# Optimization experiments

Measured on AMD Instinct MI355X. Metric: run time of the kernel, lower is better.

## Reference

```python
import jax, jax.numpy as jnp
import numpy as np

B, N, T, CIN, COUT, K, DIL = 8, 207, 12, 64, 64, 3, 1


def setup_inputs() -> dict:
    key = jax.random.key(0)
    ks = jax.random.split(key, 13)
    s = 0.05
    return {
        "X": jax.random.normal(ks[0], (B, N, T, CIN), jnp.float32),
        "wA": jax.random.normal(ks[1], (COUT, CIN, 1, K), jnp.float32) * s,
        "bA": jax.random.normal(ks[2], (COUT,), jnp.float32) * s,
        "wB": jax.random.normal(ks[3], (COUT, CIN, 1, K), jnp.float32) * s,
        "bB": jax.random.normal(ks[4], (COUT,), jnp.float32) * s,
        "wq": jax.random.normal(ks[5], (COUT // 8, COUT), jnp.float32) * s,
        "bq": jax.random.normal(ks[6], (COUT // 8,), jnp.float32) * s,
        "wk": jax.random.normal(ks[7], (COUT // 8, COUT), jnp.float32) * s,
        "bk": jax.random.normal(ks[8], (COUT // 8,), jnp.float32) * s,
        "wv": jax.random.normal(ks[9], (COUT, COUT), jnp.float32) * s,
        "bv": jax.random.normal(ks[10], (COUT,), jnp.float32) * s,
        "gamma": jax.random.normal(ks[11], (1,), jnp.float32) * 0.1,
    }


def reference(X, wA, bA, wB, bB, wq, bq, wk, bk, wv, bv, gamma):
    # X: [B, N, T, C] -> [B, C, N, T]
    x = jnp.transpose(X, (0, 3, 1, 2))
    k_size = wA.shape[-1]
    pad = (k_size - 1) * DIL  # causal left pad == pad-both + drop-right in torch code

    def causal_conv(w, b):
        y = jax.lax.conv_general_dilated(
            x, w, window_strides=(1, 1),
            padding=((0, 0), (pad, 0)),
            rhs_dilation=(1, DIL),
            dimension_numbers=("NCHW", "OIHW", "NCHW"))
        return y + b[None, :, None, None]

    A = causal_conv(wA, bA)
    Bg = causal_conv(wB, bB)
    h = A * jax.nn.sigmoid(Bg)  # [B, C, N, T]

    b_, c, w_, h_ = h.shape
    L = w_ * h_
    h2 = h.reshape(b_, c, L)  # [B, C, L]
    q = jnp.einsum("oc,bcl->bol", wq, h2) + bq[None, :, None]  # [B, C/8, L]
    kk = jnp.einsum("oc,bcl->bol", wk, h2) + bk[None, :, None]
    v = jnp.einsum("oc,bcl->bol", wv, h2) + bv[None, :, None]   # [B, C, L]

    energy = jnp.einsum("bql,bqm->blm", q, kk)  # [B, L, L]
    attn = jax.nn.softmax(energy, axis=-1)
    out = jnp.einsum("bcm,blm->bcl", v, attn).reshape(b_, c, w_, h_)
    out = gamma[0] * out + h
    return jnp.transpose(out, (0, 2, 3, 1))  # [B, N, T, C]
```

## Files before the change

### kernel.cpp

```cpp
#include <hip/hip_runtime.h>
#include <hip/hip_bf16.h>

#define Bn 8
#define Nn 207
#define Tn 12
#define Cn 64
#define Ln (Nn*Tn)
#define LP 2496
#define NT 39
#define NB 104

typedef unsigned int u32;
typedef unsigned short u16;
typedef _Float16 f16;
typedef __attribute__((ext_vector_type(4))) _Float16 half4;
typedef __attribute__((ext_vector_type(4))) float floatx4;

__device__ __forceinline__ u16 f2h(float f) { f16 h = (f16)f; return *(u16*)&h; }
__device__ __forceinline__ float h2f_lo(u32 u) { u16 x = (u16)u;        f16 h = *(f16*)&x; return (float)h; }
__device__ __forceinline__ float h2f_hi(u32 u) { u16 x = (u16)(u >> 16); f16 h = *(f16*)&x; return (float)h; }

#define W_PW   0
#define U_WVT  24576
#define F_WK   14336
#define F_WQ   14848
#define U_K    30720
#define U_Q    190464
#define U_HT   350208

__global__ __launch_bounds__(256) void prep_kernel(
    const float* __restrict__ wA, const float* __restrict__ wB,
    const float* __restrict__ wq, const float* __restrict__ wk,
    const float* __restrict__ wv, float* __restrict__ ws)
{
    u16* wsu = (u16*)ws;
    u32* wsw = (u32*)ws;
    int idx = blockIdx.x * 256 + threadIdx.x;
    if (idx < 12288) {
        int co = idx & 63, j = (idx >> 6) & 7, cig = (idx >> 9) & 7, k = idx >> 12;
        int src = (co*64 + cig*8 + j)*3 + k;
        wsw[W_PW + idx] = (u32)f2h(wA[src]) | ((u32)f2h(wB[src]) << 16);
    } else if (idx < 16384) {
        int j = idx - 12288;
        wsu[U_WVT + j] = f2h(wv[j]);
    } else if (idx < 16896) {
        int j = idx - 16384; int o = j & 7, c = j >> 3;
        ws[F_WK + j] = wk[o*Cn + c];
    } else if (idx < 17408) {
        int j = idx - 16896; int o = j & 7, c = j >> 3;
        ws[F_WQ + j] = wq[o*Cn + c];
    } else if (idx < 18944) {
        int j = idx - 17408;
        int b = j / 192, rem = j - b*192;
        int which = rem / 96, rr = rem - which*96;
        wsu[(which ? U_Q : U_K) + (size_t)b*LP*8 + Ln*8 + rr] = 0;
    } else if (idx < 25088) {
        int j = idx - 18944;
        int b = j / 768, rem = j - b*768;
        int c = rem / 12, mm = 52 + (rem - c*12);
        int ss = mm >> 4, q = (mm >> 2) & 3, i = mm & 3;
        int cs = c >> 4, rm = c & 15;
        wsu[U_HT + (size_t)b*NT*4096 + ((38*16 + ss*4 + cs)*256 + (rm*4 + q)*4 + i)] = 0;
    }
}

__global__ __launch_bounds__(256, 2) void conv_k_kernel(
    const float* __restrict__ X,
    const float* __restrict__ bA, const float* __restrict__ bB,
    const float* __restrict__ bk, const float* __restrict__ bq,
    float* __restrict__ ws, float* __restrict__ out)
{
    __shared__ u32   w_s[12288];
    __shared__ float xs[Tn*Cn];
    __shared__ float hs[Tn*Cn];
    __shared__ float wkq_s[1024];
    int b = blockIdx.x & 7;
    int n = blockIdx.x >> 3;
    int tid = threadIdx.x;

    for (int i = tid; i < 3072; i += 256)
        ((uint4*)w_s)[i] = ((const uint4*)ws)[i];
    const float* Xp = X + (size_t)(b*Nn + n)*Tn*Cn;
    for (int i = tid; i < (Tn*Cn)/4; i += 256)
        ((float4*)xs)[i] = ((const float4*)Xp)[i];
    ((float4*)wkq_s)[tid] = ((const float4*)(ws + F_WK))[tid];
    __syncthreads();

    int co = tid & 63;
    int tg = tid >> 6;
    float aA[3] = {bA[co], bA[co], bA[co]};
    float aB[3] = {bB[co], bB[co], bB[co]};
    int tb = tg*3 - 2;

    #pragma unroll 1
    for (int cig = 0; cig < 8; ++cig) {
        float xr[5][8];
        #pragma unroll
        for (int d = 0; d < 5; ++d) {
            int tp = tb + d;
            if (tp >= 0) {
                float4 xa = *(const float4*)(xs + tp*Cn + cig*8);
                float4 xb = *(const float4*)(xs + tp*Cn + cig*8 + 4);
                xr[d][0]=xa.x; xr[d][1]=xa.y; xr[d][2]=xa.z; xr[d][3]=xa.w;
                xr[d][4]=xb.x; xr[d][5]=xb.y; xr[d][6]=xb.z; xr[d][7]=xb.w;
            } else {
                #pragma unroll
                for (int j = 0; j < 8; ++j) xr[d][j] = 0.f;
            }
        }
        #pragma unroll
        for (int k = 0; k < 3; ++k) {
            #pragma unroll
            for (int j = 0; j < 8; ++j) {
                u32 p = w_s[((k*8 + cig)*8 + j)*64 + co];
                float wa = h2f_lo(p), wb = h2f_hi(p);
                #pragma unroll
                for (int tt = 0; tt < 3; ++tt) {
                    aA[tt] += xr[tt + k][j] * wa;
                    aB[tt] += xr[tt + k][j] * wb;
                }
            }
        }
    }

    #pragma unroll
    for (int tt = 0; tt < 3; ++tt) {
        int t = tg*3 + tt;
        float hv = aA[tt] * (1.f / (1.f + __expf(-aB[tt])));
        hs[t*Cn + co] = hv;
        out[((size_t)b*Ln + (size_t)n*Tn + t)*Cn + co] = hv;
    }
    __syncthreads();

    if (tid < 96) {
        int r = tid >> 3, o = tid & 7;
        float acc = bk[o];
        for (int c = 0; c < Cn; ++c) acc += hs[r*Cn + c] * wkq_s[c*8 + o];
        ((u16*)ws)[U_K + (size_t)b*LP*8 + ((size_t)n*Tn + r)*8 + o] = f2h(acc);
    } else if (tid < 192) {
        int r = (tid - 96) >> 3, o = tid & 7;
        float acc = bq[o];
        for (int c = 0; c < Cn; ++c) acc += hs[r*Cn + c] * wkq_s[512 + c*8 + o];
        ((u16*)ws)[U_Q + (size_t)b*LP*8 + ((size_t)n*Tn + r)*8 + o] = f2h(acc);
    }
    {
        int jj = tid >> 6, c = tid & 63;
        if (jj < 3) {
            int m = n*Tn + 4*jj;
            int tile = m >> 6, mloc = m & 63;
            int ss = mloc >> 4, q = (mloc >> 2) & 3;
            int cs = c >> 4, rm = c & 15;
            u32 p0 = ((u32)f2h(hs[(4*jj+1)*Cn + c]) << 16) | f2h(hs[(4*jj+0)*Cn + c]);
            u32 p1 = ((u32)f2h(hs[(4*jj+3)*Cn + c]) << 16) | f2h(hs[(4*jj+2)*Cn + c]);
            u16* ht = (u16*)ws + U_HT + (size_t)b*NT*4096
                    + ((tile*16 + ss*4 + cs)*256 + (rm*4 + q)*4);
            *(uint2*)ht = make_uint2(p0, p1);
        }
    }
}

__global__ __launch_bounds__(256, 3) void attn_kernel(
    const float* __restrict__ gamma, const float* __restrict__ bv,
    const float* __restrict__ ws, float* __restrict__ out)
{
    __shared__ float part[4*64*24];
    __shared__ float den_part[4][32];

    int b  = blockIdx.x & 7;
    int nb = blockIdx.x >> 3;
    int R0 = nb*24;
    int tid = threadIdx.x;
    int lane = tid & 63;
    int w = tid >> 6;
    int rm = lane & 15;
    int quad = lane >> 4;

    const u16* wsu = (const u16*)ws;
    const u16* kb = wsu + U_K  + (size_t)b*LP*8;
    const u16* qb = wsu + U_Q  + (size_t)b*LP*8;
    const u16* hb = wsu + U_HT + (size_t)b*NT*4096;

    half4 qf0, qf1;
    {
        uint2 u0 = make_uint2(0, 0), u1 = make_uint2(0, 0);
        int r0 = R0 + rm;       if (r0 >= LP) r0 = LP - 1;
        int r1 = R0 + 16 + rm;  if (r1 >= LP) r1 = LP - 1;
        if (quad < 2) {
            u0 = *(const uint2*)(qb + (size_t)r0*8 + 4*quad);
            u1 = *(const uint2*)(qb + (size_t)r1*8 + 4*quad);
        }
        qf0 = *(half4*)&u0; qf1 = *(half4*)&u1;
    }

    floatx4 acc[4][2];
    #pragma unroll
    for (int cs = 0; cs < 4; ++cs)
        #pragma unroll
        for (int g = 0; g < 2; ++g) acc[cs][g] = (floatx4){0.f, 0.f, 0.f, 0.f};
    float dsum0 = 0.f, dsum1 = 0.f;

    uint2 k0_0,k0_1,k0_2,k0_3, k1_0,k1_1,k1_2,k1_3;
    uint2 h0_0,h0_1,h0_2,h0_3,h0_4,h0_5,h0_6,h0_7,h0_8,h0_9,h0_10,h0_11,h0_12,h0_13,h0_14,h0_15;
    uint2 h1_0,h1_1,h1_2,h1_3,h1_4,h1_5,h1_6,h1_7,h1_8,h1_9,h1_10,h1_11,h1_12,h1_13,h1_14,h1_15;

#define LDK(kt, SS) ((quad < 2) ? *(const uint2*)((kt) + ((SS)*16 + rm)*8 + 4*quad) : make_uint2(0,0))
#define LDH(ht, IDX) (*(const uint2*)((ht) + (IDX)*256 + lane*4))

#define LOADT(B, T) {                                                          \
    int tc = ((T) < NT) ? (T) : (NT-1);                                        \
    const u16* kt_ = kb + (size_t)tc*512;                                      \
    const u16* ht_ = hb + (size_t)tc*4096;                                     \
    k##B##_0 = LDK(kt_, 0); k##B##_1 = LDK(kt_, 1);                            \
    k##B##_2 = LDK(kt_, 2); k##B##_3 = LDK(kt_, 3);                            \
    h##B##_0  = LDH(ht_, 0);  h##B##_1  = LDH(ht_, 1);                         \
    h##B##_2  = LDH(ht_, 2);  h##B##_3  = LDH(ht_, 3);                         \
    h##B##_4  = LDH(ht_, 4);  h##B##_5  = LDH(ht_, 5);                         \
    h##B##_6  = LDH(ht_, 6);  h##B##_7  = LDH(ht_, 7);                         \
    h##B##_8  = LDH(ht_, 8);  h##B##_9  = LDH(ht_, 9);                         \
    h##B##_10 = LDH(ht_, 10); h##B##_11 = LDH(ht_, 11);                        \
    h##B##_12 = LDH(ht_, 12); h##B##_13 = LDH(ht_, 13);                        \
    h##B##_14 = LDH(ht_, 14); h##B##_15 = LDH(ht_, 15);                        \
}

#define COMPSS(KR, HA, HB_, HC, HD, T, SS) {                                   \
    half4 kf = *(half4*)&KR;                                                   \
    floatx4 s0 = {0.f,0.f,0.f,0.f}, s1 = {0.f,0.f,0.f,0.f};                    \
    s0 = __builtin_amdgcn_mfma_f32_16x16x16f16(kf, qf0, s0, 0, 0, 0);          \
    s1 = __builtin_amdgcn_mfma_f32_16x16x16f16(kf, qf1, s1, 0, 0, 0);          \
    half4 e0, e1;                                                              \
    int mb = (T)*64 + (SS)*16 + 4*quad;                                        \
    _Pragma("unroll")                                                          \
    for (int i_ = 0; i_ < 4; ++i_) {                                           \
        float ev0 = (mb + i_ < Ln) ? __expf(s0[i_]) : 0.f;                     \
        float ev1 = (mb + i_ < Ln) ? __expf(s1[i_]) : 0.f;                     \
        dsum0 += ev0; dsum1 += ev1;                                            \
        e0[i_] = (f16)ev0; e1[i_] = (f16)ev1;                                  \
    }                                                                          \
    half4 a0_ = *(half4*)&HA, a1_ = *(half4*)&HB_, a2_ = *(half4*)&HC, a3_ = *(half4*)&HD; \
    acc[0][0] = __builtin_amdgcn_mfma_f32_16x16x16f16(a0_, e0, acc[0][0], 0, 0, 0); \
    acc[0][1] = __builtin_amdgcn_mfma_f32_16x16x16f16(a0_, e1, acc[0][1], 0, 0, 0); \
    acc[1][0] = __builtin_amdgcn_mfma_f32_16x16x16f16(a1_, e0, acc[1][0], 0, 0, 0); \
    acc[1][1] = __builtin_amdgcn_mfma_f32_16x16x16f16(a1_, e1, acc[1][1], 0, 0, 0); \
    acc[2][0] = __builtin_amdgcn_mfma_f32_16x16x16f16(a2_, e0, acc[2][0], 0, 0, 0); \
    acc[2][1] = __builtin_amdgcn_mfma_f32_16x16x16f16(a2_, e1, acc[2][1], 0, 0, 0); \
    acc[3][0] = __builtin_amdgcn_mfma_f32_16x16x16f16(a3_, e0, acc[3][0], 0, 0, 0); \
    acc[3][1] = __builtin_amdgcn_mfma_f32_16x16x16f16(a3_, e1, acc[3][1], 0, 0, 0); \
}

#define COMPT(B, T) {                                                          \
    COMPSS(k##B##_0, h##B##_0,  h##B##_1,  h##B##_2,  h##B##_3,  T, 0)         \
    COMPSS(k##B##_1, h##B##_4,  h##B##_5,  h##B##_6,  h##B##_7,  T, 1)         \
    COMPSS(k##B##_2, h##B##_8,  h##B##_9,  h##B##_10, h##B##_11, T, 2)         \
    COMPSS(k##B##_3, h##B##_12, h##B##_13, h##B##_14, h##B##_15, T, 3)         \
}

    LOADT(0, w)
    for (int i = 0; i < 5; ++i) {
        int t0 = w + 8*i;
        LOADT(1, t0 + 4)
        COMPT(0, t0)
        LOADT(0, t0 + 8)
        COMPT(1, t0 + 4)
    }
#undef LOADT
#undef COMPT
#undef COMPSS
#undef LDK
#undef LDH

    {
        float s_ = dsum0;
        s_ += __shfl_xor(s_, 16, 64);
        s_ += __shfl_xor(s_, 32, 64);
        if (quad == 0) den_part[w][rm] = s_;
        float t_ = dsum1;
        t_ += __shfl_xor(t_, 16, 64);
        t_ += __shfl_xor(t_, 32, 64);
        if (quad == 0) den_part[w][16 + rm] = t_;
    }

    float* pw = part + w*1536;
    #pragma unroll
    for (int cs = 0; cs < 4; ++cs) {
        #pragma unroll
        for (int i = 0; i < 4; ++i)
            pw[(cs*16 + quad*4 + i)*24 + rm] = acc[cs][0][i];
        if (rm < 8) {
            #pragma unroll
            for (int i = 0; i < 4; ++i)
                pw[(cs*16 + quad*4 + i)*24 + 16 + rm] = acc[cs][1][i];
        }
    }
    __syncthreads();

    for (int j = tid; j < 1536; j += 256)
        part[j] = part[j] + part[1536 + j] + part[3072 + j] + part[4608 + j];
    __syncthreads();

    int o = tid & 63, rq = tid >> 6;
    float gam = gamma[0];
    float bvo = bv[o];
    const u16* wvr = wsu + U_WVT + o*64;
    uint4 wvu[8];
    #pragma unroll
    for (int x = 0; x < 8; ++x) wvu[x] = *(const uint4*)(wvr + x*8);
    #pragma unroll
    for (int rr = 0; rr < 6; ++rr) {
        int r = rq*6 + rr;
        int row = R0 + r;
        if (row < Ln) {
            float den = den_part[0][r] + den_part[1][r] + den_part[2][r] + den_part[3][r];
            float p = 0.f;
            #pragma unroll
            for (int x = 0; x < 8; ++x) {
                const f16* hh = (const f16*)&wvu[x];
                #pragma unroll
                for (int i = 0; i < 8; ++i)
                    p += (float)hh[i] * part[(x*8 + i)*24 + r];
            }
            size_t gi = ((size_t)b*Ln + row)*64 + o;
            out[gi] = gam*(bvo + p/den) + out[gi];
        }
    }
}

extern "C" void kernel_launch(void* const* d_in, const int* in_sizes, int n_in,
                              void* d_out, int out_size, void* d_ws, size_t ws_size,
                              hipStream_t stream) {
    const float* X     = (const float*)d_in[0];
    const float* wA    = (const float*)d_in[1];
    const float* bA    = (const float*)d_in[2];
    const float* wB    = (const float*)d_in[3];
    const float* bB    = (const float*)d_in[4];
    const float* wq    = (const float*)d_in[5];
    const float* bq    = (const float*)d_in[6];
    const float* wk    = (const float*)d_in[7];
    const float* bk    = (const float*)d_in[8];
    const float* wv    = (const float*)d_in[9];
    const float* bv    = (const float*)d_in[10];
    const float* gamma = (const float*)d_in[11];
    float* out = (float*)d_out;
    float* ws  = (float*)d_ws;

    prep_kernel<<<98, 256, 0, stream>>>(wA, wB, wq, wk, wv, ws);
    conv_k_kernel<<<Bn*Nn, 256, 0, stream>>>(X, bA, bB, bk, bq, ws, out);
    attn_kernel<<<Bn*NB, 256, 0, stream>>>(gamma, bv, ws, out);
}
```

Measured before the change: 158.6 us.

## Stream conv weights from global, drop LDS staging, widen attention blocks to 8 waves

The conv kernel no longer copies the full 48KB packed weight table into shared memory per block. It reads weights directly from global or cache in a per-thread contiguous layout, double-buffered across input-channel groups, and the prep kernel is reordered to write that layout. This lowers LDS use so the launch bound can allow 4 blocks per CU. The attention kernel moves to 512 threads (8 waves), each wave covering 5 key tiles instead of 10, with a wider partial-sum reduction in shared memory; this raises parallelism per block but uses more LDS and adds reduction work.

```diff
diff --git a/kernel.cpp b/kernel.cpp
--- a/kernel.cpp
+++ b/kernel.cpp
@@ -37,9 +37,10 @@
     u32* wsw = (u32*)ws;
     int idx = blockIdx.x * 256 + threadIdx.x;
     if (idx < 12288) {
-        int co = idx & 63, j = (idx >> 6) & 7, cig = (idx >> 9) & 7, k = idx >> 12;
+        int j = idx & 7, co = (idx >> 3) & 63, cig = (idx >> 9) & 7, k = idx >> 12;
         int src = (co*64 + cig*8 + j)*3 + k;
-        wsw[W_PW + idx] = (u32)f2h(wA[src]) | ((u32)f2h(wB[src]) << 16);
+        wsw[W_PW + ((k*8 + cig)*64 + co)*8 + j] =
+            (u32)f2h(wA[src]) | ((u32)f2h(wB[src]) << 16);
     } else if (idx < 16384) {
         int j = idx - 12288;
         wsu[U_WVT + j] = f2h(wv[j]);
@@ -64,13 +65,12 @@
     }
 }
 
-__global__ __launch_bounds__(256, 2) void conv_k_kernel(
+__global__ __launch_bounds__(256, 4) void conv_k_kernel(
     const float* __restrict__ X,
     const float* __restrict__ bA, const float* __restrict__ bB,
     const float* __restrict__ bk, const float* __restrict__ bq,
     float* __restrict__ ws, float* __restrict__ out)
 {
-    __shared__ u32   w_s[12288];
     __shared__ float xs[Tn*Cn];
     __shared__ float hs[Tn*Cn];
     __shared__ float wkq_s[1024];
@@ -78,8 +78,6 @@
     int n = blockIdx.x >> 3;
     int tid = threadIdx.x;
 
-    for (int i = tid; i < 3072; i += 256)
-        ((uint4*)w_s)[i] = ((const uint4*)ws)[i];
     const float* Xp = X + (size_t)(b*Nn + n)*Tn*Cn;
     for (int i = tid; i < (Tn*Cn)/4; i += 256)
         ((float4*)xs)[i] = ((const float4*)Xp)[i];
@@ -91,37 +89,64 @@
     float aA[3] = {bA[co], bA[co], bA[co]};
     float aB[3] = {bB[co], bB[co], bB[co]};
     int tb = tg*3 - 2;
-
+    const uint4* wp4 = (const uint4*)((const u32*)ws + W_PW);
+
+    uint4 p00, p01, p02, p03, p04, p05;
+    uint4 p10, p11, p12, p13, p14, p15;
+
+#define LOADW(V0,V1,V2,V3,V4,V5, CIG) {                    \
+    V0 = wp4[(0*8 + (CIG))*128 + co*2 + 0];                \
+    V1 = wp4[(0*8 + (CIG))*128 + co*2 + 1];                \
+    V2 = wp4[(1*8 + (CIG))*128 + co*2 + 0];                \
+    V3 = wp4[(1*8 + (CIG))*128 + co*2 + 1];                \
+    V4 = wp4[(2*8 + (CIG))*128 + co*2 + 0];                \
+    V5 = wp4[(2*8 + (CIG))*128 + co*2 + 1];                \
+}
+
+#define COMPK(K, WH0, WH1) {                               \
+    u32 uu[8] = {WH0.x, WH0.y, WH0.z, WH0.w,               \
+                 WH1.x, WH1.y, WH1.z, WH1.w};              \
+    _Pragma("unroll")                                      \
+    for (int j = 0; j < 8; ++j) {                          \
+        float wav = h2f_lo(uu[j]), wbv = h2f_hi(uu[j]);    \
+        _Pragma("unroll")                                  \
+        for (int tt = 0; tt < 3; ++tt) {                   \
+            aA[tt] += xr[tt + K][j] * wav;                 \
+            aB[tt] += xr[tt + K][j] * wbv;                 \
+        }                                                  \
+    }                                                      \
+}
+
+#define COMPC(CIG, V0,V1,V2,V3,V4,V5) {                    \
+    float xr[5][8];                                        \
+    _Pragma("unroll")                                      \
+    for (int d = 0; d < 5; ++d) {                          \
+        int tp = tb + d;                                   \
+        if (tp >= 0) {                                     \
+            float4 xa = *(const float4*)(xs + tp*Cn + (CIG)*8);     \
+            float4 xb = *(const float4*)(xs + tp*Cn + (CIG)*8 + 4); \
+            xr[d][0]=xa.x; xr[d][1]=xa.y; xr[d][2]=xa.z; xr[d][3]=xa.w; \
+            xr[d][4]=xb.x; xr[d][5]=xb.y; xr[d][6]=xb.z; xr[d][7]=xb.w; \
+        } else {                                           \
+            _Pragma("unroll")                              \
+            for (int j = 0; j < 8; ++j) xr[d][j] = 0.f;    \
+        }                                                  \
+    }                                                      \
+    COMPK(0, V0, V1) COMPK(1, V2, V3) COMPK(2, V4, V5)     \
+}
+
+    LOADW(p00,p01,p02,p03,p04,p05, 0)
     #pragma unroll 1
-    for (int cig = 0; cig < 8; ++cig) {
-        float xr[5][8];
-        #pragma unroll
-        for (int d = 0; d < 5; ++d) {
-            int tp = tb + d;
-            if (tp >= 0) {
-                float4 xa = *(const float4*)(xs + tp*Cn + cig*8);
-                float4 xb = *(const float4*)(xs + tp*Cn + cig*8 + 4);
-                xr[d][0]=xa.x; xr[d][1]=xa.y; xr[d][2]=xa.z; xr[d][3]=xa.w;
-                xr[d][4]=xb.x; xr[d][5]=xb.y; xr[d][6]=xb.z; xr[d][7]=xb.w;
-            } else {
-                #pragma unroll
-                for (int j = 0; j < 8; ++j) xr[d][j] = 0.f;
-            }
-        }
-        #pragma unroll
-        for (int k = 0; k < 3; ++k) {
-            #pragma unroll
-            for (int j = 0; j < 8; ++j) {
-                u32 p = w_s[((k*8 + cig)*8 + j)*64 + co];
-                float wa = h2f_lo(p), wb = h2f_hi(p);
-                #pragma unroll
-                for (int tt = 0; tt < 3; ++tt) {
-                    aA[tt] += xr[tt + k][j] * wa;
-                    aB[tt] += xr[tt + k][j] * wb;
-                }
-            }
-        }
-    }
+    for (int c2 = 0; c2 < 4; ++c2) {
+        int cig0 = 2*c2;
+        LOADW(p10,p11,p12,p13,p14,p15, cig0 + 1)
+        COMPC(cig0, p00,p01,p02,p03,p04,p05)
+        if (c2 < 3) LOADW(p00,p01,p02,p03,p04,p05, cig0 + 2)
+        COMPC(cig0 + 1, p10,p11,p12,p13,p14,p15)
+    }
+#undef LOADW
+#undef COMPK
+#undef COMPC
 
     #pragma unroll
     for (int tt = 0; tt < 3; ++tt) {
@@ -150,21 +175,21 @@
             int tile = m >> 6, mloc = m & 63;
             int ss = mloc >> 4, q = (mloc >> 2) & 3;
             int cs = c >> 4, rm = c & 15;
-            u32 p0 = ((u32)f2h(hs[(4*jj+1)*Cn + c]) << 16) | f2h(hs[(4*jj+0)*Cn + c]);
-            u32 p1 = ((u32)f2h(hs[(4*jj+3)*Cn + c]) << 16) | f2h(hs[(4*jj+2)*Cn + c]);
+            u32 q0 = ((u32)f2h(hs[(4*jj+1)*Cn + c]) << 16) | f2h(hs[(4*jj+0)*Cn + c]);
+            u32 q1 = ((u32)f2h(hs[(4*jj+3)*Cn + c]) << 16) | f2h(hs[(4*jj+2)*Cn + c]);
             u16* ht = (u16*)ws + U_HT + (size_t)b*NT*4096
                     + ((tile*16 + ss*4 + cs)*256 + (rm*4 + q)*4);
-            *(uint2*)ht = make_uint2(p0, p1);
+            *(uint2*)ht = make_uint2(q0, q1);
         }
     }
 }
 
-__global__ __launch_bounds__(256, 3) void attn_kernel(
+__global__ __launch_bounds__(512, 4) void attn_kernel(
     const float* __restrict__ gamma, const float* __restrict__ bv,
     const float* __restrict__ ws, float* __restrict__ out)
 {
-    __shared__ float part[4*64*24];
-    __shared__ float den_part[4][32];
+    __shared__ float part[8*1536];
+    __shared__ float den_part[8][32];
 
     int b  = blockIdx.x & 7;
     int nb = blockIdx.x >> 3;
@@ -255,13 +280,15 @@
 }
 
     LOADT(0, w)
-    for (int i = 0; i < 5; ++i) {
-        int t0 = w + 8*i;
-        LOADT(1, t0 + 4)
-        COMPT(0, t0)
-        LOADT(0, t0 + 8)
-        COMPT(1, t0 + 4)
-    }
+    LOADT(1, w + 8)
+    COMPT(0, w)
+    LOADT(0, w + 16)
+    COMPT(1, w + 8)
+    LOADT(1, w + 24)
+    COMPT(0, w + 16)
+    LOADT(0, w + 32)
+    COMPT(1, w + 24)
+    COMPT(0, w + 32)
 #undef LOADT
 #undef COMPT
 #undef COMPSS
@@ -293,8 +320,9 @@
     }
     __syncthreads();
 
-    for (int j = tid; j < 1536; j += 256)
-        part[j] = part[j] + part[1536 + j] + part[3072 + j] + part[4608 + j];
+    for (int j = tid; j < 1536; j += 512)
+        part[j] = ((part[j]          + part[1536   + j]) + (part[2*1536 + j] + part[3*1536 + j]))
+                + ((part[4*1536 + j] + part[5*1536 + j]) + (part[6*1536 + j] + part[7*1536 + j]));
     __syncthreads();
 
     int o = tid & 63, rq = tid >> 6;
@@ -305,11 +333,12 @@
     #pragma unroll
     for (int x = 0; x < 8; ++x) wvu[x] = *(const uint4*)(wvr + x*8);
     #pragma unroll
-    for (int rr = 0; rr < 6; ++rr) {
-        int r = rq*6 + rr;
+    for (int rr = 0; rr < 3; ++rr) {
+        int r = rq*3 + rr;
         int row = R0 + r;
         if (row < Ln) {
-            float den = den_part[0][r] + den_part[1][r] + den_part[2][r] + den_part[3][r];
+            float den = ((den_part[0][r] + den_part[1][r]) + (den_part[2][r] + den_part[3][r]))
+                      + ((den_part[4][r] + den_part[5][r]) + (den_part[6][r] + den_part[7][r]));
             float p = 0.f;
             #pragma unroll
             for (int x = 0; x < 8; ++x) {
@@ -344,5 +373,5 @@
 
     prep_kernel<<<98, 256, 0, stream>>>(wA, wB, wq, wk, wv, ws);
     conv_k_kernel<<<Bn*Nn, 256, 0, stream>>>(X, bA, bB, bk, bq, ws, out);
-    attn_kernel<<<Bn*NB, 256, 0, stream>>>(gamma, bv, ws, out);
-}
+    attn_kernel<<<Bn*NB, 512, 0, stream>>>(gamma, bv, ws, out);
+}
```

Measured after the change: 221.2 us. 39.5% more time.

## Stream attention value tiles into LDS with async global_load_lds double buffering

Applied to the files above, without the earlier changes.

Instead of holding two full H tiles in registers, each wave now copies its H tiles asynchronously from global memory into a private double-buffered LDS region with global_load_lds. It waits on vmcnt so one tile is computed while the next loads, and the main loop is fully unrolled. The aim is to free the large block of VGPRs the H tiles used, raise occupancy (launch bounds hinted at 4 blocks), and overlap loads with MFMA work. In exchange, LDS use per block rises to about 64KB, which may cap how many blocks fit per CU. It also adds LDS read traffic and depends on the hand-written vmcnt waits to order the async writes against LDS reads.

```diff
diff --git a/kernel.cpp b/kernel.cpp
--- a/kernel.cpp
+++ b/kernel.cpp
@@ -19,6 +19,9 @@
 __device__ __forceinline__ u16 f2h(float f) { f16 h = (f16)f; return *(u16*)&h; }
 __device__ __forceinline__ float h2f_lo(u32 u) { u16 x = (u16)u;        f16 h = *(f16*)&x; return (float)h; }
 __device__ __forceinline__ float h2f_hi(u32 u) { u16 x = (u16)(u >> 16); f16 h = *(f16*)&x; return (float)h; }
+
+#define AS1(p) ((const __attribute__((address_space(1))) void*)(unsigned long long)(p))
+#define AS3(p) ((__attribute__((address_space(3))) void*)(unsigned int)(unsigned long long)(p))
 
 #define W_PW   0
 #define U_WVT  24576
@@ -150,20 +153,20 @@
             int tile = m >> 6, mloc = m & 63;
             int ss = mloc >> 4, q = (mloc >> 2) & 3;
             int cs = c >> 4, rm = c & 15;
-            u32 p0 = ((u32)f2h(hs[(4*jj+1)*Cn + c]) << 16) | f2h(hs[(4*jj+0)*Cn + c]);
-            u32 p1 = ((u32)f2h(hs[(4*jj+3)*Cn + c]) << 16) | f2h(hs[(4*jj+2)*Cn + c]);
+            u32 q0 = ((u32)f2h(hs[(4*jj+1)*Cn + c]) << 16) | f2h(hs[(4*jj+0)*Cn + c]);
+            u32 q1 = ((u32)f2h(hs[(4*jj+3)*Cn + c]) << 16) | f2h(hs[(4*jj+2)*Cn + c]);
             u16* ht = (u16*)ws + U_HT + (size_t)b*NT*4096
                     + ((tile*16 + ss*4 + cs)*256 + (rm*4 + q)*4);
-            *(uint2*)ht = make_uint2(p0, p1);
-        }
-    }
-}
-
-__global__ __launch_bounds__(256, 3) void attn_kernel(
+            *(uint2*)ht = make_uint2(q0, q1);
+        }
+    }
+}
+
+__global__ __launch_bounds__(256, 4) void attn_kernel(
     const float* __restrict__ gamma, const float* __restrict__ bv,
     const float* __restrict__ ws, float* __restrict__ out)
 {
-    __shared__ float part[4*64*24];
+    __shared__ __align__(16) unsigned char lds_pool[65536];
     __shared__ float den_part[4][32];
 
     int b  = blockIdx.x & 7;
@@ -174,6 +177,7 @@
     int w = tid >> 6;
     int rm = lane & 15;
     int quad = lane >> 4;
+    unsigned wbase = (unsigned)w * 16384u;
 
     const u16* wsu = (const u16*)ws;
     const u16* kb = wsu + U_K  + (size_t)b*LP*8;
@@ -200,29 +204,32 @@
     float dsum0 = 0.f, dsum1 = 0.f;
 
     uint2 k0_0,k0_1,k0_2,k0_3, k1_0,k1_1,k1_2,k1_3;
-    uint2 h0_0,h0_1,h0_2,h0_3,h0_4,h0_5,h0_6,h0_7,h0_8,h0_9,h0_10,h0_11,h0_12,h0_13,h0_14,h0_15;
-    uint2 h1_0,h1_1,h1_2,h1_3,h1_4,h1_5,h1_6,h1_7,h1_8,h1_9,h1_10,h1_11,h1_12,h1_13,h1_14,h1_15;
 
 #define LDK(kt, SS) ((quad < 2) ? *(const uint2*)((kt) + ((SS)*16 + rm)*8 + 4*quad) : make_uint2(0,0))
-#define LDH(ht, IDX) (*(const uint2*)((ht) + (IDX)*256 + lane*4))
-
-#define LOADT(B, T) {                                                          \
+
+#define DMA(P, T) {                                                            \
+    int tc = ((T) < NT) ? (T) : (NT-1);                                        \
+    const unsigned char* g_ = (const unsigned char*)(hb + (size_t)tc*4096);    \
+    _Pragma("unroll")                                                          \
+    for (int c_ = 0; c_ < 8; ++c_)                                             \
+        __builtin_amdgcn_global_load_lds(                                      \
+            AS1(g_ + c_*1024 + lane*16),                                       \
+            AS3(lds_pool + wbase + (P)*8192 + c_*1024), 16, 0, 0);             \
+}
+
+#define KLOAD(B, T) {                                                          \
     int tc = ((T) < NT) ? (T) : (NT-1);                                        \
     const u16* kt_ = kb + (size_t)tc*512;                                      \
-    const u16* ht_ = hb + (size_t)tc*4096;                                     \
     k##B##_0 = LDK(kt_, 0); k##B##_1 = LDK(kt_, 1);                            \
     k##B##_2 = LDK(kt_, 2); k##B##_3 = LDK(kt_, 3);                            \
-    h##B##_0  = LDH(ht_, 0);  h##B##_1  = LDH(ht_, 1);                         \
-    h##B##_2  = LDH(ht_, 2);  h##B##_3  = LDH(ht_, 3);                         \
-    h##B##_4  = LDH(ht_, 4);  h##B##_5  = LDH(ht_, 5);                         \
-    h##B##_6  = LDH(ht_, 6);  h##B##_7  = LDH(ht_, 7);                         \
-    h##B##_8  = LDH(ht_, 8);  h##B##_9  = LDH(ht_, 9);                         \
-    h##B##_10 = LDH(ht_, 10); h##B##_11 = LDH(ht_, 11);                        \
-    h##B##_12 = LDH(ht_, 12); h##B##_13 = LDH(ht_, 13);                        \
-    h##B##_14 = LDH(ht_, 14); h##B##_15 = LDH(ht_, 15);                        \
-}
-
-#define COMPSS(KR, HA, HB_, HC, HD, T, SS) {                                   \
+}
+
+#define WAITV12 asm volatile("s_waitcnt vmcnt(12)" ::: "memory");
+#define WAITV0  asm volatile("s_waitcnt vmcnt(0)"  ::: "memory");
+
+#define LDSH(P, IDX) (*(const uint2*)(lds_pool + wbase + (P)*8192 + (IDX)*512 + lane*8))
+
+#define COMPSS(P, KR, T, SS) {                                                 \
     half4 kf = *(half4*)&KR;                                                   \
     floatx4 s0 = {0.f,0.f,0.f,0.f}, s1 = {0.f,0.f,0.f,0.f};                    \
     s0 = __builtin_amdgcn_mfma_f32_16x16x16f16(kf, qf0, s0, 0, 0, 0);          \
@@ -236,7 +243,10 @@
         dsum0 += ev0; dsum1 += ev1;                                            \
         e0[i_] = (f16)ev0; e1[i_] = (f16)ev1;                                  \
     }                                                                          \
-    half4 a0_ = *(half4*)&HA, a1_ = *(half4*)&HB_, a2_ = *(half4*)&HC, a3_ = *(half4*)&HD; \
+    uint2 au0 = LDSH(P, (SS)*4 + 0), au1 = LDSH(P, (SS)*4 + 1);                \
+    uint2 au2 = LDSH(P, (SS)*4 + 2), au3 = LDSH(P, (SS)*4 + 3);                \
+    half4 a0_ = *(half4*)&au0, a1_ = *(half4*)&au1;                            \
+    half4 a2_ = *(half4*)&au2, a3_ = *(half4*)&au3;                            \
     acc[0][0] = __builtin_amdgcn_mfma_f32_16x16x16f16(a0_, e0, acc[0][0], 0, 0, 0); \
     acc[0][1] = __builtin_amdgcn_mfma_f32_16x16x16f16(a0_, e1, acc[0][1], 0, 0, 0); \
     acc[1][0] = __builtin_amdgcn_mfma_f32_16x16x16f16(a1_, e0, acc[1][0], 0, 0, 0); \
@@ -247,26 +257,31 @@
     acc[3][1] = __builtin_amdgcn_mfma_f32_16x16x16f16(a3_, e1, acc[3][1], 0, 0, 0); \
 }
 
-#define COMPT(B, T) {                                                          \
-    COMPSS(k##B##_0, h##B##_0,  h##B##_1,  h##B##_2,  h##B##_3,  T, 0)         \
-    COMPSS(k##B##_1, h##B##_4,  h##B##_5,  h##B##_6,  h##B##_7,  T, 1)         \
-    COMPSS(k##B##_2, h##B##_8,  h##B##_9,  h##B##_10, h##B##_11, T, 2)         \
-    COMPSS(k##B##_3, h##B##_12, h##B##_13, h##B##_14, h##B##_15, T, 3)         \
-}
-
-    LOADT(0, w)
-    for (int i = 0; i < 5; ++i) {
-        int t0 = w + 8*i;
-        LOADT(1, t0 + 4)
-        COMPT(0, t0)
-        LOADT(0, t0 + 8)
-        COMPT(1, t0 + 4)
-    }
-#undef LOADT
+#define COMPT(P, KB, T) {                                                      \
+    COMPSS(P, k##KB##_0, T, 0)                                                 \
+    COMPSS(P, k##KB##_1, T, 1)                                                 \
+    COMPSS(P, k##KB##_2, T, 2)                                                 \
+    COMPSS(P, k##KB##_3, T, 3)                                                 \
+}
+
+    DMA(0, w)      KLOAD(0, w)
+    DMA(1, w + 4)  KLOAD(1, w + 4)   WAITV12  COMPT(0, 0, w)
+    DMA(0, w + 8)  KLOAD(0, w + 8)   WAITV12  COMPT(1, 1, w + 4)
+    DMA(1, w + 12) KLOAD(1, w + 12)  WAITV12  COMPT(0, 0, w + 8)
+    DMA(0, w + 16) KLOAD(0, w + 16)  WAITV12  COMPT(1, 1, w + 12)
+    DMA(1, w + 20) KLOAD(1, w + 20)  WAITV12  COMPT(0, 0, w + 16)
+    DMA(0, w + 24) KLOAD(0, w + 24)  WAITV12  COMPT(1, 1, w + 20)
+    DMA(1, w + 28) KLOAD(1, w + 28)  WAITV12  COMPT(0, 0, w + 24)
+    DMA(0, w + 32) KLOAD(0, w + 32)  WAITV12  COMPT(1, 1, w + 28)
+    DMA(1, w + 36) KLOAD(1, w + 36)  WAITV12  COMPT(0, 0, w + 32)
+    WAITV0                                    COMPT(1, 1, w + 36)
+
+#undef DMA
+#undef KLOAD
 #undef COMPT
 #undef COMPSS
+#undef LDSH
 #undef LDK
-#undef LDH
 
     {
         float s_ = dsum0;
@@ -279,7 +294,8 @@
         if (quad == 0) den_part[w][16 + rm] = t_;
     }
 
-    float* pw = part + w*1536;
+    float* part = (float*)lds_pool;
+    float* pw = part + w*4096;
     #pragma unroll
     for (int cs = 0; cs < 4; ++cs) {
         #pragma unroll
@@ -294,7 +310,7 @@
     __syncthreads();
 
     for (int j = tid; j < 1536; j += 256)
-        part[j] = part[j] + part[1536 + j] + part[3072 + j] + part[4608 + j];
+        part[j] = part[j] + part[4096 + j] + part[8192 + j] + part[12288 + j];
     __syncthreads();
 
     int o = tid & 63, rq = tid >> 6;
```

Result: slower. 188.0 us (+18.5%).
